# Kernel tuning notes

Measured on AMD Instinct MI355X. Metric: run time of the kernel, lower is better.

The kernel has to match this reference:

```python
import jax, jax.numpy as jnp
import numpy as np

D_MODEL = 1792
BB = 256
I = D_MODEL + BB  # inner_dim = 2048


def setup_inputs() -> dict:
    key = jax.random.key(0)
    ks = jax.random.split(key, 10)
    s = 1.0 / np.sqrt(I)  # PyTorch LSTM default init range
    u = lambda k, shape: jax.random.uniform(k, shape, jnp.float32, -s, s)
    return {
        "x": jax.random.normal(ks[0], (6, D_MODEL), jnp.float32),
        "y": jax.random.normal(ks[1], (5, BB), jnp.float32),
        "Wih5": u(ks[2], (5, 4 * I, I)),
        "Whh5": u(ks[3], (5, 4 * I, I)),
        "bih5": u(ks[4], (5, 4 * I)),
        "bhh5": u(ks[5], (5, 4 * I)),
        "WihF": u(ks[6], (4 * I, D_MODEL)),
        "WhhF": u(ks[7], (4 * I, I)),
        "bihF": u(ks[8], (4 * I,)),
        "bhhF": u(ks[9], (4 * I,)),
    }


def _cell(h, c, xt, Wih, Whh, bih, bhh):
    # PyTorch LSTM cell: gates in i, f, g, o order
    g = Wih @ xt + bih + Whh @ h + bhh  # (4I,)
    i, f, gg, o = jnp.split(g, 4)
    c = jax.nn.sigmoid(f) * c + jax.nn.sigmoid(i) * jnp.tanh(gg)
    h = jax.nn.sigmoid(o) * jnp.tanh(c)
    return h, c


def reference(x, y, Wih5, Whh5, bih5, bhh5, WihF, WhhF, bihF, bhhF):
    # inpt: (5, inner_dim) = concat of first 5 frames and 5 gts
    inpt = jnp.concatenate([x[:-1], y], axis=1)
    h0 = jnp.zeros((I,), x.dtype)
    c0 = jnp.zeros((I,), x.dtype)

    def step(carry, xs):
        h, c = carry
        xt, Wih, Whh, bih, bhh = xs
        return _cell(h, c, xt, Wih, Whh, bih, bhh), None

    # 5 sequential single-step LSTM cells (distinct weights), fused via scan
    (h, c), _ = jax.lax.scan(step, (h0, c0), (inpt, Wih5, Whh5, bih5, bhh5))
    # final LSTM consumes the last frame (d_model input)
    h, c = _cell(h, c, x[-1], WihF, WhhF, bihF, bhhF)
    return h[-BB:]
```

## Files before the change

kernel.cpp:

```cpp
#include <hip/hip_runtime.h>
#include <cmath>

#define D_MODEL 1792
#define BB      256
#define II      2048
#define FOURI   8192

__device__ __forceinline__ float sigm(float v) { return 1.0f / (1.0f + expf(-v)); }

__device__ __forceinline__ float waveReduce(float s) {
    #pragma unroll
    for (int off = 32; off > 0; off >>= 1) s += __shfl_down(s, off, 64);
    return s;
}

__device__ __forceinline__ float dotConcat(const float* __restrict__ wrow,
                                           const float* __restrict__ xt,
                                           const float* __restrict__ yt,
                                           int lane) {
    float sum = 0.f;
    #pragma unroll
    for (int p = 0; p < 8; ++p) {
        const int j = p * 256 + lane * 4;
        float4 w = *(const float4*)(wrow + j);
        float4 v = (p < 7) ? *(const float4*)(xt + j)
                           : *(const float4*)(yt + (j - D_MODEL));
        sum += w.x * v.x + w.y * v.y + w.z * v.z + w.w * v.w;
    }
    return sum;
}

__device__ __forceinline__ float dotH(const float* __restrict__ wrow,
                                      const float* __restrict__ h,
                                      int lane) {
    float sum = 0.f;
    #pragma unroll
    for (int p = 0; p < 8; ++p) {
        const int j = p * 256 + lane * 4;
        float4 w = *(const float4*)(wrow + j);
        float4 v = *(const float4*)(h + j);
        sum += w.x * v.x + w.y * v.y + w.z * v.z + w.w * v.w;
    }
    return sum;
}

__global__ __launch_bounds__(256) void step0_kernel(
    const float* __restrict__ x,
    const float* __restrict__ y,
    const float* __restrict__ Wih5,
    const float* __restrict__ bih5,
    const float* __restrict__ bhh5,
    float* __restrict__ h_out,
    float* __restrict__ c_out,
    float* __restrict__ gih_out)
{
    const int wave = threadIdx.x >> 6;
    const int lane = threadIdx.x & 63;

    if (blockIdx.x < 2048) {
        __shared__ float partial[4];
        const int r = blockIdx.x;
        const float* wrow = Wih5 + ((size_t)wave * II + r) * (size_t)II;
        float sum = dotConcat(wrow, x, y, lane);
        sum = waveReduce(sum);
        if (lane == 0)
            partial[wave] = sum + bih5[wave * II + r] + bhh5[wave * II + r];
        __syncthreads();
        if (threadIdx.x == 0) {
            const float gi = partial[0], gg = partial[2], go = partial[3];
            const float cc = sigm(gi) * tanhf(gg);
            c_out[r] = cc;
            h_out[r] = sigm(go) * tanhf(cc);
        }
    } else {
        const int u = blockIdx.x - 2048;
        const float* wrow = Wih5 + ((size_t)FOURI + (size_t)wave * II + u) * (size_t)II;
        float sum = dotConcat(wrow, x + D_MODEL, y + BB, lane);
        sum = waveReduce(sum);
        if (lane == 0)
            gih_out[wave * II + u] =
                sum + bih5[FOURI + wave * II + u] + bhh5[FOURI + wave * II + u];
    }
}

__global__ __launch_bounds__(256) void mid_kernel(
    const float* __restrict__ Whh,
    const float* __restrict__ gih_in,
    const float* __restrict__ h_in,
    float* __restrict__ h_out,
    float* __restrict__ c,
    const float* __restrict__ WihN,
    const float* __restrict__ bihN,
    const float* __restrict__ bhhN,
    const float* __restrict__ xN,
    const float* __restrict__ yN,
    float* __restrict__ gih_out)
{
    const int wave = threadIdx.x >> 6;
    const int lane = threadIdx.x & 63;

    if (blockIdx.x < 2048) {
        __shared__ float partial[4];
        const int r = blockIdx.x;
        const float* wrow = Whh + ((size_t)wave * II + r) * (size_t)II;
        float sum = dotH(wrow, h_in, lane);
        sum = waveReduce(sum);
        if (lane == 0) partial[wave] = sum + gih_in[wave * II + r];
        __syncthreads();
        if (threadIdx.x == 0) {
            const float gi = partial[0], gf = partial[1], gg = partial[2], go = partial[3];
            const float cc = sigm(gf) * c[r] + sigm(gi) * tanhf(gg);
            c[r] = cc;
            h_out[r] = sigm(go) * tanhf(cc);
        }
    } else {
        const int u = blockIdx.x - 2048;
        const float* wrow = WihN + ((size_t)wave * II + u) * (size_t)II;
        float sum = dotConcat(wrow, xN, yN, lane);
        sum = waveReduce(sum);
        if (lane == 0)
            gih_out[wave * II + u] = sum + bihN[wave * II + u] + bhhN[wave * II + u];
    }
}

__global__ __launch_bounds__(256) void mid4_kernel(
    const float* __restrict__ Whh,
    const float* __restrict__ gih_in,
    const float* __restrict__ h_in,
    float* __restrict__ h_out,
    float* __restrict__ c,
    const float* __restrict__ WihF,
    const float* __restrict__ bihF,
    const float* __restrict__ bhhF,
    const float* __restrict__ x5,
    float* __restrict__ gihF_out)
{
    const int wave = threadIdx.x >> 6;
    const int lane = threadIdx.x & 63;

    if (blockIdx.x < 2048) {
        __shared__ float partial[4];
        const int r = blockIdx.x;
        const float* wrow = Whh + ((size_t)wave * II + r) * (size_t)II;
        float sum = dotH(wrow, h_in, lane);
        sum = waveReduce(sum);
        if (lane == 0) partial[wave] = sum + gih_in[wave * II + r];
        __syncthreads();
        if (threadIdx.x == 0) {
            const float gi = partial[0], gf = partial[1], gg = partial[2], go = partial[3];
            const float cc = sigm(gf) * c[r] + sigm(gi) * tanhf(gg);
            c[r] = cc;
            h_out[r] = sigm(go) * tanhf(cc);
        }
    } else {
        const int u = blockIdx.x - 2048;
        const int r = wave * II + D_MODEL + u;
        const float* wrow = WihF + (size_t)r * (size_t)D_MODEL;
        float sum = 0.f;
        #pragma unroll
        for (int p = 0; p < 7; ++p) {
            const int j = p * 256 + lane * 4;
            float4 w = *(const float4*)(wrow + j);
            float4 v = *(const float4*)(x5 + j);
            sum += w.x * v.x + w.y * v.y + w.z * v.z + w.w * v.w;
        }
        sum = waveReduce(sum);
        if (lane == 0)
            gihF_out[wave * BB + u] = sum + bihF[r] + bhhF[r];
    }
}

__global__ __launch_bounds__(256) void final_kernel(
    const float* __restrict__ WhhF,
    const float* __restrict__ gihF,
    const float* __restrict__ h_in,
    const float* __restrict__ c,
    float* __restrict__ out)
{
    __shared__ float partial[4];
    const int k    = blockIdx.x;
    const int r    = D_MODEL + k;
    const int wave = threadIdx.x >> 6;
    const int lane = threadIdx.x & 63;

    const float* wrow = WhhF + ((size_t)wave * II + r) * (size_t)II;
    float sum = dotH(wrow, h_in, lane);
    sum = waveReduce(sum);
    if (lane == 0) partial[wave] = sum + gihF[wave * BB + k];
    __syncthreads();
    if (threadIdx.x == 0) {
        const float gi = partial[0], gf = partial[1], gg = partial[2], go = partial[3];
        const float cc = sigm(gf) * c[r] + sigm(gi) * tanhf(gg);
        out[k] = sigm(go) * tanhf(cc);
    }
}

extern "C" void kernel_launch(void* const* d_in, const int* in_sizes, int n_in,
                              void* d_out, int out_size, void* d_ws, size_t ws_size,
                              hipStream_t stream) {
    const float* x    = (const float*)d_in[0];
    const float* y    = (const float*)d_in[1];
    const float* Wih5 = (const float*)d_in[2];
    const float* Whh5 = (const float*)d_in[3];
    const float* bih5 = (const float*)d_in[4];
    const float* bhh5 = (const float*)d_in[5];
    const float* WihF = (const float*)d_in[6];
    const float* WhhF = (const float*)d_in[7];
    const float* bihF = (const float*)d_in[8];
    const float* bhhF = (const float*)d_in[9];
    float* out = (float*)d_out;

    float* ws   = (float*)d_ws;
    float* gihA = ws;
    float* gihB = gihA + FOURI;
    float* gihF = gihB + FOURI;
    float* hA   = gihF + 1024;
    float* hB   = hA + II;
    float* cbuf = hB + II;

    const size_t WOFF = (size_t)FOURI * II;

    step0_kernel<<<4096, 256, 0, stream>>>(x, y, Wih5, bih5, bhh5, hA, cbuf, gihA);

    mid_kernel<<<4096, 256, 0, stream>>>(
        Whh5 + 1 * WOFF, gihA, hA, hB, cbuf,
        Wih5 + 2 * WOFF, bih5 + 2 * FOURI, bhh5 + 2 * FOURI,
        x + 2 * D_MODEL, y + 2 * BB, gihB);

    mid_kernel<<<4096, 256, 0, stream>>>(
        Whh5 + 2 * WOFF, gihB, hB, hA, cbuf,
        Wih5 + 3 * WOFF, bih5 + 3 * FOURI, bhh5 + 3 * FOURI,
        x + 3 * D_MODEL, y + 3 * BB, gihA);

    mid_kernel<<<4096, 256, 0, stream>>>(
        Whh5 + 3 * WOFF, gihA, hA, hB, cbuf,
        Wih5 + 4 * WOFF, bih5 + 4 * FOURI, bhh5 + 4 * FOURI,
        x + 4 * D_MODEL, y + 4 * BB, gihB);

    mid4_kernel<<<2304, 256, 0, stream>>>(
        Whh5 + 4 * WOFF, gihB, hB, hA, cbuf,
        WihF, bihF, bhhF, x + 5 * D_MODEL, gihF);

    final_kernel<<<BB, 256, 0, stream>>>(WhhF, gihF, hA, cbuf, out);
}
```

Before: 121.0 us.

## Stage input vectors in LDS and skip unused forget-gate rows in step 0

Each block now copies its input vector (h or the concatenated x/y frame) into shared memory once, and the per-row dot products read it from LDS instead of global memory. Step 0 no longer computes the forget-gate rows, which are useless because the initial cell state is zero. That wave instead computes one next-step input-gate row, cutting the step-0 grid from 4096 to 3584 blocks. Input-projection blocks now do four consecutive rows per block, one per wave, with a remapped row index. The cost is an extra staging pass and a block barrier per block, on a workload that is bound by streaming the weights.

```diff
diff --git a/kernel.cpp b/kernel.cpp
--- a/kernel.cpp
+++ b/kernel.cpp
@@ -14,184 +14,199 @@
     return s;
 }
 
-__device__ __forceinline__ float dotConcat(const float* __restrict__ wrow,
-                                           const float* __restrict__ xt,
-                                           const float* __restrict__ yt,
-                                           int lane) {
-    float sum = 0.f;
+__device__ __forceinline__ void stage2048(float* dst, const float* src, int tid) {
+    float4* d4 = (float4*)dst;
+    const float4* s4 = (const float4*)src;
+    d4[tid]       = s4[tid];
+    d4[tid + 256] = s4[tid + 256];
+    __syncthreads();
+}
+
+__device__ __forceinline__ void stageConcat(float* dst, const float* xt,
+                                            const float* yt, int tid) {
+    float4* d4 = (float4*)dst;
+    const float4* x4 = (const float4*)xt;
+    const float4* y4 = (const float4*)yt;
+    int i = tid;
+    d4[i] = (i < 448) ? x4[i] : y4[i - 448];
+    i = tid + 256;
+    d4[i] = (i < 448) ? x4[i] : y4[i - 448];
+    __syncthreads();
+}
+
+__device__ __forceinline__ float dotLds(const float* __restrict__ w,
+                                        const float* hs, int lane) {
+    float s = 0.f;
     #pragma unroll
     for (int p = 0; p < 8; ++p) {
         const int j = p * 256 + lane * 4;
-        float4 w = *(const float4*)(wrow + j);
-        float4 v = (p < 7) ? *(const float4*)(xt + j)
-                           : *(const float4*)(yt + (j - D_MODEL));
-        sum += w.x * v.x + w.y * v.y + w.z * v.z + w.w * v.w;
-    }
-    return sum;
-}
-
-__device__ __forceinline__ float dotH(const float* __restrict__ wrow,
-                                      const float* __restrict__ h,
-                                      int lane) {
-    float sum = 0.f;
-    #pragma unroll
-    for (int p = 0; p < 8; ++p) {
-        const int j = p * 256 + lane * 4;
-        float4 w = *(const float4*)(wrow + j);
-        float4 v = *(const float4*)(h + j);
-        sum += w.x * v.x + w.y * v.y + w.z * v.z + w.w * v.w;
-    }
-    return sum;
-}
-
-__global__ __launch_bounds__(256) void step0_kernel(
-    const float* __restrict__ x,
-    const float* __restrict__ y,
+        float4 a = *(const float4*)(w + j);
+        float4 b = *(const float4*)(hs + j);
+        s += a.x * b.x + a.y * b.y + a.z * b.z + a.w * b.w;
+    }
+    return s;
+}
+
+__global__ __launch_bounds__(256) void k0(
+    const float* __restrict__ x, const float* __restrict__ y,
     const float* __restrict__ Wih5,
-    const float* __restrict__ bih5,
-    const float* __restrict__ bhh5,
-    float* __restrict__ h_out,
-    float* __restrict__ c_out,
-    float* __restrict__ gih_out)
-{
-    const int wave = threadIdx.x >> 6;
-    const int lane = threadIdx.x & 63;
-
-    if (blockIdx.x < 2048) {
-        __shared__ float partial[4];
-        const int r = blockIdx.x;
-        const float* wrow = Wih5 + ((size_t)wave * II + r) * (size_t)II;
-        float sum = dotConcat(wrow, x, y, lane);
-        sum = waveReduce(sum);
+    const float* __restrict__ bih5, const float* __restrict__ bhh5,
+    float* __restrict__ h0, float* __restrict__ c0, float* __restrict__ gih1)
+{
+    __shared__ float buf[II];
+    __shared__ float partial[4];
+    const int tid = threadIdx.x, wave = tid >> 6, lane = tid & 63;
+    const int b = blockIdx.x;
+
+    if (b < II) {
+        stageConcat(buf, x, y, tid);
+        if (wave != 1) {
+            const float* wr = Wih5 + ((size_t)wave * II + b) * (size_t)II;
+            float s = dotLds(wr, buf, lane);
+            s = waveReduce(s);
+            if (lane == 0)
+                partial[wave] = s + bih5[wave * II + b] + bhh5[wave * II + b];
+        } else {
+            const float* wr = Wih5 + ((size_t)FOURI + b) * (size_t)II;
+            const float* xt = x + D_MODEL;
+            const float* yt = y + BB;
+            float s = 0.f;
+            #pragma unroll
+            for (int p = 0; p < 8; ++p) {
+                const int j = p * 256 + lane * 4;
+                float4 a = *(const float4*)(wr + j);
+                float4 v = (p < 7) ? *(const float4*)(xt + j)
+                                   : *(const float4*)(yt + (j - D_MODEL));
+                s += a.x * v.x + a.y * v.y + a.z * v.z + a.w * v.w;
+            }
+            s = waveReduce(s);
+            if (lane == 0)
+                gih1[b] = s + bih5[FOURI + b] + bhh5[FOURI + b];
+        }
+        __syncthreads();
+        if (tid == 0) {
+            const float cc = sigm(partial[0]) * tanhf(partial[2]);
+            c0[b] = cc;
+            h0[b] = sigm(partial[3]) * tanhf(cc);
+        }
+    } else {
+        stageConcat(buf, x + D_MODEL, y + BB, tid);
+        const int row = II + (b - II) * 4 + wave;
+        const float* wr = Wih5 + ((size_t)FOURI + row) * (size_t)II;
+        float s = dotLds(wr, buf, lane);
+        s = waveReduce(s);
         if (lane == 0)
-            partial[wave] = sum + bih5[wave * II + r] + bhh5[wave * II + r];
-        __syncthreads();
-        if (threadIdx.x == 0) {
-            const float gi = partial[0], gg = partial[2], go = partial[3];
-            const float cc = sigm(gi) * tanhf(gg);
-            c_out[r] = cc;
-            h_out[r] = sigm(go) * tanhf(cc);
-        }
-    } else {
-        const int u = blockIdx.x - 2048;
-        const float* wrow = Wih5 + ((size_t)FOURI + (size_t)wave * II + u) * (size_t)II;
-        float sum = dotConcat(wrow, x + D_MODEL, y + BB, lane);
-        sum = waveReduce(sum);
-        if (lane == 0)
-            gih_out[wave * II + u] =
-                sum + bih5[FOURI + wave * II + u] + bhh5[FOURI + wave * II + u];
-    }
-}
-
-__global__ __launch_bounds__(256) void mid_kernel(
+            gih1[row] = s + bih5[FOURI + row] + bhh5[FOURI + row];
+    }
+}
+
+__global__ __launch_bounds__(256) void kmid(
     const float* __restrict__ Whh,
-    const float* __restrict__ gih_in,
-    const float* __restrict__ h_in,
-    float* __restrict__ h_out,
+    const float* __restrict__ gih_t,
+    const float* __restrict__ h_in, float* __restrict__ h_out,
     float* __restrict__ c,
     const float* __restrict__ WihN,
-    const float* __restrict__ bihN,
-    const float* __restrict__ bhhN,
-    const float* __restrict__ xN,
-    const float* __restrict__ yN,
-    float* __restrict__ gih_out)
-{
-    const int wave = threadIdx.x >> 6;
-    const int lane = threadIdx.x & 63;
-
-    if (blockIdx.x < 2048) {
-        __shared__ float partial[4];
-        const int r = blockIdx.x;
-        const float* wrow = Whh + ((size_t)wave * II + r) * (size_t)II;
-        float sum = dotH(wrow, h_in, lane);
-        sum = waveReduce(sum);
-        if (lane == 0) partial[wave] = sum + gih_in[wave * II + r];
-        __syncthreads();
-        if (threadIdx.x == 0) {
-            const float gi = partial[0], gf = partial[1], gg = partial[2], go = partial[3];
-            const float cc = sigm(gf) * c[r] + sigm(gi) * tanhf(gg);
-            c[r] = cc;
-            h_out[r] = sigm(go) * tanhf(cc);
+    const float* __restrict__ bihN, const float* __restrict__ bhhN,
+    const float* __restrict__ xN, const float* __restrict__ yN,
+    float* __restrict__ gihN)
+{
+    __shared__ float buf[II];
+    __shared__ float partial[4];
+    const int tid = threadIdx.x, wave = tid >> 6, lane = tid & 63;
+    const int b = blockIdx.x;
+
+    if (b < II) {
+        stage2048(buf, h_in, tid);
+        const float* wr = Whh + ((size_t)wave * II + b) * (size_t)II;
+        float s = dotLds(wr, buf, lane);
+        s = waveReduce(s);
+        if (lane == 0) partial[wave] = s + gih_t[wave * II + b];
+        __syncthreads();
+        if (tid == 0) {
+            const float cc = sigm(partial[1]) * c[b]
+                           + sigm(partial[0]) * tanhf(partial[2]);
+            c[b] = cc;
+            h_out[b] = sigm(partial[3]) * tanhf(cc);
         }
     } else {
-        const int u = blockIdx.x - 2048;
-        const float* wrow = WihN + ((size_t)wave * II + u) * (size_t)II;
-        float sum = dotConcat(wrow, xN, yN, lane);
-        sum = waveReduce(sum);
-        if (lane == 0)
-            gih_out[wave * II + u] = sum + bihN[wave * II + u] + bhhN[wave * II + u];
-    }
-}
-
-__global__ __launch_bounds__(256) void mid4_kernel(
-    const float* __restrict__ Whh,
-    const float* __restrict__ gih_in,
-    const float* __restrict__ h_in,
-    float* __restrict__ h_out,
+        stageConcat(buf, xN, yN, tid);
+        const int row = (b - II) * 4 + wave;
+        const float* wr = WihN + (size_t)row * (size_t)II;
+        float s = dotLds(wr, buf, lane);
+        s = waveReduce(s);
+        if (lane == 0) gihN[row] = s + bihN[row] + bhhN[row];
+    }
+}
+
+__global__ __launch_bounds__(256) void k4(
+    const float* __restrict__ Whh4, const float* __restrict__ gih4,
+    const float* __restrict__ h_in, float* __restrict__ h_out,
     float* __restrict__ c,
-    const float* __restrict__ WihF,
-    const float* __restrict__ bihF,
-    const float* __restrict__ bhhF,
-    const float* __restrict__ x5,
-    float* __restrict__ gihF_out)
-{
-    const int wave = threadIdx.x >> 6;
-    const int lane = threadIdx.x & 63;
-
-    if (blockIdx.x < 2048) {
-        __shared__ float partial[4];
-        const int r = blockIdx.x;
-        const float* wrow = Whh + ((size_t)wave * II + r) * (size_t)II;
-        float sum = dotH(wrow, h_in, lane);
-        sum = waveReduce(sum);
-        if (lane == 0) partial[wave] = sum + gih_in[wave * II + r];
-        __syncthreads();
-        if (threadIdx.x == 0) {
-            const float gi = partial[0], gf = partial[1], gg = partial[2], go = partial[3];
-            const float cc = sigm(gf) * c[r] + sigm(gi) * tanhf(gg);
-            c[r] = cc;
-            h_out[r] = sigm(go) * tanhf(cc);
+    const float* __restrict__ WihF, const float* __restrict__ bihF,
+    const float* __restrict__ bhhF, const float* __restrict__ x5,
+    float* __restrict__ gihF)
+{
+    __shared__ float buf[II];
+    __shared__ float partial[4];
+    const int tid = threadIdx.x, wave = tid >> 6, lane = tid & 63;
+    const int b = blockIdx.x;
+
+    if (b < II) {
+        stage2048(buf, h_in, tid);
+        const float* wr = Whh4 + ((size_t)wave * II + b) * (size_t)II;
+        float s = dotLds(wr, buf, lane);
+        s = waveReduce(s);
+        if (lane == 0) partial[wave] = s + gih4[wave * II + b];
+        __syncthreads();
+        if (tid == 0) {
+            const float cc = sigm(partial[1]) * c[b]
+                           + sigm(partial[0]) * tanhf(partial[2]);
+            c[b] = cc;
+            h_out[b] = sigm(partial[3]) * tanhf(cc);
         }
     } else {
-        const int u = blockIdx.x - 2048;
-        const int r = wave * II + D_MODEL + u;
-        const float* wrow = WihF + (size_t)r * (size_t)D_MODEL;
-        float sum = 0.f;
+        float4* d4 = (float4*)buf;
+        const float4* s4 = (const float4*)x5;
+        d4[tid] = (tid < 448) ? s4[tid] : make_float4(0.f, 0.f, 0.f, 0.f);
+        if (tid < 192) d4[tid + 256] = s4[tid + 256];
+        __syncthreads();
+        const int j = (b - II) * 4 + wave;
+        const int row = (j >> 8) * II + D_MODEL + (j & 255);
+        const float* wr = WihF + (size_t)row * (size_t)D_MODEL;
+        float s = 0.f;
         #pragma unroll
         for (int p = 0; p < 7; ++p) {
-            const int j = p * 256 + lane * 4;
-            float4 w = *(const float4*)(wrow + j);
-            float4 v = *(const float4*)(x5 + j);
-            sum += w.x * v.x + w.y * v.y + w.z * v.z + w.w * v.w;
-        }
-        sum = waveReduce(sum);
-        if (lane == 0)
-            gihF_out[wave * BB + u] = sum + bihF[r] + bhhF[r];
-    }
-}
-
-__global__ __launch_bounds__(256) void final_kernel(
-    const float* __restrict__ WhhF,
-    const float* __restrict__ gihF,
-    const float* __restrict__ h_in,
-    const float* __restrict__ c,
+            const int jj = p * 256 + lane * 4;
+            float4 a = *(const float4*)(wr + jj);
+            float4 v = *(const float4*)(buf + jj);
+            s += a.x * v.x + a.y * v.y + a.z * v.z + a.w * v.w;
+        }
+        s = waveReduce(s);
+        if (lane == 0) gihF[j] = s + bihF[row] + bhhF[row];
+    }
+}
+
+__global__ __launch_bounds__(256) void k5(
+    const float* __restrict__ WhhF, const float* __restrict__ gihF,
+    const float* __restrict__ h_in, const float* __restrict__ c,
     float* __restrict__ out)
 {
-    __shared__ float partial[4];
-    const int k    = blockIdx.x;
-    const int r    = D_MODEL + k;
-    const int wave = threadIdx.x >> 6;
-    const int lane = threadIdx.x & 63;
-
-    const float* wrow = WhhF + ((size_t)wave * II + r) * (size_t)II;
-    float sum = dotH(wrow, h_in, lane);
-    sum = waveReduce(sum);
-    if (lane == 0) partial[wave] = sum + gihF[wave * BB + k];
+    __shared__ float buf[II];
+    __shared__ float partial[4];
+    const int tid = threadIdx.x, wave = tid >> 6, lane = tid & 63;
+    const int b = blockIdx.x;
+
+    stage2048(buf, h_in, tid);
+    const int r = D_MODEL + b;
+    const float* wr = WhhF + ((size_t)wave * II + r) * (size_t)II;
+    float s = dotLds(wr, buf, lane);
+    s = waveReduce(s);
+    if (lane == 0) partial[wave] = s + gihF[wave * BB + b];
     __syncthreads();
-    if (threadIdx.x == 0) {
-        const float gi = partial[0], gf = partial[1], gg = partial[2], go = partial[3];
-        const float cc = sigm(gf) * c[r] + sigm(gi) * tanhf(gg);
-        out[k] = sigm(go) * tanhf(cc);
+    if (tid == 0) {
+        const float cc = sigm(partial[1]) * c[r]
+                       + sigm(partial[0]) * tanhf(partial[2]);
+        out[b] = sigm(partial[3]) * tanhf(cc);
     }
 }
 
@@ -220,26 +235,26 @@
 
     const size_t WOFF = (size_t)FOURI * II;
 
-    step0_kernel<<<4096, 256, 0, stream>>>(x, y, Wih5, bih5, bhh5, hA, cbuf, gihA);
-
-    mid_kernel<<<4096, 256, 0, stream>>>(
+    k0<<<3584, 256, 0, stream>>>(x, y, Wih5, bih5, bhh5, hA, cbuf, gihA);
+
+    kmid<<<4096, 256, 0, stream>>>(
         Whh5 + 1 * WOFF, gihA, hA, hB, cbuf,
         Wih5 + 2 * WOFF, bih5 + 2 * FOURI, bhh5 + 2 * FOURI,
         x + 2 * D_MODEL, y + 2 * BB, gihB);
 
-    mid_kernel<<<4096, 256, 0, stream>>>(
+    kmid<<<4096, 256, 0, stream>>>(
         Whh5 + 2 * WOFF, gihB, hB, hA, cbuf,
         Wih5 + 3 * WOFF, bih5 + 3 * FOURI, bhh5 + 3 * FOURI,
         x + 3 * D_MODEL, y + 3 * BB, gihA);
 
-    mid_kernel<<<4096, 256, 0, stream>>>(
+    kmid<<<4096, 256, 0, stream>>>(
         Whh5 + 3 * WOFF, gihA, hA, hB, cbuf,
         Wih5 + 4 * WOFF, bih5 + 4 * FOURI, bhh5 + 4 * FOURI,
         x + 4 * D_MODEL, y + 4 * BB, gihB);
 
-    mid4_kernel<<<2304, 256, 0, stream>>>(
+    k4<<<2304, 256, 0, stream>>>(
         Whh5 + 4 * WOFF, gihB, hB, hA, cbuf,
         WihF, bihF, bhhF, x + 5 * D_MODEL, gihF);
 
-    final_kernel<<<BB, 256, 0, stream>>>(WhhF, gihF, hA, cbuf, out);
-}
+    k5<<<BB, 256, 0, stream>>>(WhhF, gihF, hA, cbuf, out);
+}
```

Result: no change. 122.3 us (+1.1%).
